# Optimization experiments

Measured on AMD Instinct MI355X. Metric: run time of the kernel, lower is better.

## Reference

```python
import jax, jax.numpy as jnp
import numpy as np

SR = 44100
LOWEST_HZ = 55.0
N_FRAMES = 100
L_ORDER = 5                       # l_filter_order
NC = L_ORDER + 1                  # num_coefficients
NA = L_ORDER + 2                  # num_active_indexes
V = int(SR // LOWEST_HZ) + NA     # coeff_vector_size = 808
N_SAMPLES = 44100


def _nat_cubic_spline_eval(y, t_out):
    """Natural cubic spline through y (n_knots, d) on uniform knots in [0,1],
    evaluated at t_out (T,). Returns (T, d)."""
    n, d = y.shape
    h = 1.0 / (n - 1)
    # second derivatives M: natural BC -> M[0] = M[n-1] = 0, tridiagonal solve
    rhs = 6.0 * (y[2:] - 2.0 * y[1:-1] + y[:-2]) / h        # (n-2, d)
    T = (jnp.diag(jnp.full((n - 2,), 4.0 * h))
         + jnp.diag(jnp.full((n - 3,), h), 1)
         + jnp.diag(jnp.full((n - 3,), h), -1))
    M_in = jnp.linalg.solve(T, rhs)
    M = jnp.concatenate([jnp.zeros((1, d), y.dtype), M_in, jnp.zeros((1, d), y.dtype)])
    idx = jnp.clip((t_out / h).astype(jnp.int32), 0, n - 2)
    f = (t_out - idx.astype(y.dtype) * h)[:, None]          # fractional offset
    y0, y1 = y[idx], y[idx + 1]
    M0, M1 = M[idx], M[idx + 1]
    bcoef = (y1 - y0) / h - h * (2.0 * M0 + M1) / 6.0
    ccoef = 0.5 * M0
    dcoef = (M1 - M0) / (6.0 * h)
    return y0 + f * (bcoef + f * (ccoef + f * dcoef))


def _sample_wise_lpc(x, a):
    """Time-varying all-pole filter: y[t] = x[t] - sum_i a[t, i] * y[t-1-i].
    x: (T,), a: (T, p) -> y: (T,)."""
    p = a.shape[1]

    def step(hist, inp):
        xt, at = inp
        yt = xt - jnp.dot(at, hist)
        hist = jnp.concatenate([yt[None], hist[:-1]])
        return hist, yt

    _, y = jax.lax.scan(step, jnp.zeros((p,), x.dtype), (x, a))
    return y


def setup_inputs() -> dict:
    key = jax.random.key(0)
    k1, k2, k3, k4 = jax.random.split(key, 4)
    # delay in samples, ~[300, 500] -> f0 in [88, 147] Hz, safely inside V=808
    delay_len_frames = 300.0 + 200.0 * jax.random.uniform(k1, (N_FRAMES,), dtype=jnp.float32)
    raw_gain = jnp.full((1,), 2.5, jnp.float32)             # sigmoid -> ~0.924 loop gain
    # raw coeffs uniform in (-2, 0) like the torch init
    raw_coeff_frames = -2.0 * jax.random.uniform(k2, (N_FRAMES, NC), dtype=jnp.float32)
    excitation = jax.random.normal(k3, (N_SAMPLES,), dtype=jnp.float32)
    exc_coefficients = 0.01 * jax.random.normal(k4, (1, N_SAMPLES, 1), dtype=jnp.float32)
    return {"delay_len_frames": delay_len_frames, "raw_gain": raw_gain,
            "raw_coeff_frames": raw_coeff_frames, "excitation": excitation,
            "exc_coefficients": exc_coefficients, "n_samples": N_SAMPLES}


def reference(delay_len_frames, raw_gain, raw_coeff_frames, excitation,
              exc_coefficients, n_samples):
    # constrained, normalized loop-filter coefficients per frame
    gain = jax.nn.sigmoid(raw_gain)                          # (1,)
    sig = jax.nn.sigmoid(raw_coeff_frames)                   # (F, NC)
    b_frames = sig / jnp.sum(sig, -1, keepdims=True) * gain

    # upsample delay + coeffs jointly with one natural cubic spline
    params = jnp.concatenate([delay_len_frames[:, None], b_frames], axis=1)  # (F, NC+1)
    t_out = jnp.linspace(0.0, 1.0, n_samples)
    up = _nat_cubic_spline_eval(params, t_out)               # (T, NC+1)
    delay, b = up[:, 0], up[:, 1:]

    z = jnp.floor(delay).astype(jnp.int32)                   # integer delay
    alfa = delay - jnp.floor(delay)                          # fractional part

    # scatter-build the per-sample sparse filter rows into dense A (T, V)
    cols = z[:, None] + jnp.arange(NA)[None, :]              # (T, NA)
    first = (-(1.0 - alfa) * b[:, 0])[:, None]
    mid = -(alfa[:, None] * b[:, :-1] + (1.0 - alfa)[:, None] * b[:, 1:])
    last = (-alfa * b[:, -1])[:, None]
    vals = jnp.concatenate([first, mid, last], axis=1)       # (T, NA)
    A = jnp.zeros((n_samples, V), jnp.float32).at[
        jnp.arange(n_samples)[:, None], cols].set(vals)

    # excitation shaping (order-1 time-varying all-pole), then KS string loop
    x = _sample_wise_lpc(excitation, exc_coefficients[0])
    y = _sample_wise_lpc(x, A)
    return y
```

## Files before the change

### kernel.cpp

```cpp
#include <hip/hip_runtime.h>

#define NSMP 44100
#define NKNOT 100
#define NIV  (NKNOT - 1)
#define NCC 6
#define NAA 7
#define RING 1024
#define NTH 320
#define SEG ((NSMP + NTH - 1) / NTH)
#define GW 8
#define WS_NEEDED ((size_t)NSMP * 32)

__device__ __forceinline__ float sigm(float x) { return 1.0f / (1.0f + expf(-x)); }

__device__ __forceinline__ void lean_barrier() {
    asm volatile("s_waitcnt lgkmcnt(0)" ::: "memory");
    __builtin_amdgcn_s_barrier();
    __builtin_amdgcn_sched_barrier(0);
}

__device__ __forceinline__ void prep_spline(
    const float* __restrict__ dlf, const float* __restrict__ rg,
    const float* __restrict__ rcf,
    float (*P)[NAA], float (*M)[NAA], float* CPs, float* IMs,
    float4 (*CO)[8], int* s_minz, int tid)
{
    const float H = 1.0f / 99.0f;
    if (tid < NKNOT) {
        float g = sigm(rg[0]);
        float s[NCC];
        float sum = 0.0f;
#pragma unroll
        for (int j = 0; j < NCC; ++j) { s[j] = sigm(rcf[tid * NCC + j]); sum += s[j]; }
        P[tid][0] = dlf[tid];
#pragma unroll
        for (int j = 0; j < NCC; ++j) P[tid][j + 1] = s[j] / sum * g;
    }
    if (tid < NKNOT - 2) {
        float cp = 0.25f;
        int n = tid; if (n > 10) n = 10;
        for (int k = 0; k < n; ++k) cp = 1.0f / (4.0f - cp);
        CPs[tid] = cp;
    }
    __syncthreads();
    if (tid >= 1 && tid < NKNOT - 2) IMs[tid] = 99.0f / (4.0f - CPs[tid - 1]);
    __syncthreads();
    if (tid < NAA) {
        int c = tid;
        float rhs0  = 6.0f * (P[2][c] - 2.0f * P[1][c] + P[0][c]) * 99.0f;
        float dprev = rhs0 * 24.75f;
        M[1][c] = dprev;
        for (int i = 1; i < NKNOT - 2; ++i) {
            float rhs = 6.0f * (P[i + 2][c] - 2.0f * P[i + 1][c] + P[i][c]) * 99.0f;
            float d   = (rhs - H * dprev) * IMs[i];
            M[i + 1][c] = d;
            dprev = d;
        }
        float nxt = M[NKNOT - 2][c];
        for (int i = NKNOT - 4; i >= 0; --i) {
            float v = M[i + 1][c] - CPs[i] * nxt;
            M[i + 1][c] = v;
            nxt = v;
        }
        M[0][c] = 0.0f;
        M[NKNOT - 1][c] = 0.0f;
    }
    __syncthreads();
    if (tid < NIV) {
        float lb = fminf(P[tid][0], P[tid + 1][0])
                 - (H * H * 0.125f) * fmaxf(fabsf(M[tid][0]), fabsf(M[tid + 1][0]));
        atomicMin(s_minz, (int)floorf(lb));
    }
    for (int iv = tid; iv < NIV; iv += blockDim.x) {
#pragma unroll
        for (int c = 0; c < NAA; ++c) {
            float y0 = P[iv][c], y1 = P[iv + 1][c];
            float m0 = M[iv][c], m1 = M[iv + 1][c];
            float b  = (y1 - y0) * 99.0f - H * (2.0f * m0 + m1) * (1.0f / 6.0f);
            CO[iv][c] = make_float4(y0, b, 0.5f * m0, (m1 - m0) * (99.0f / 6.0f));
        }
    }
    __syncthreads();
}


__global__ __launch_bounds__(NTH, 1) void diffks_fast(
    const float* __restrict__ dlf, const float* __restrict__ rg,
    const float* __restrict__ rcf, const float* __restrict__ exc,
    const float* __restrict__ ecoef, float* __restrict__ out,
    float4* __restrict__ recA, float4* __restrict__ recB)
{
    __shared__ float  P[NKNOT][NAA];
    __shared__ float  M[NKNOT][NAA];
    __shared__ float4 CO[NIV][8];
    __shared__ float  ring[2 * RING];
    __shared__ float  CPs[NKNOT - 2];
    __shared__ float  IMs[NKNOT - 2];
    __shared__ float  wpS[NTH / 64], wqS[NTH / 64];
    __shared__ int    s_minz;

    const int tid  = threadIdx.x;
    const int lane = tid & 63;
    const int wav  = tid >> 6;
    const float H   = 1.0f / 99.0f;
    const float INV = 1.0f / (float)(NSMP - 1);

    if (tid == 0) s_minz = 0x7fffffff;
    for (int i = tid; i < 2 * RING; i += NTH) ring[i] = 0.0f;

    prep_spline(dlf, rg, rcf, P, M, CPs, IMs, CO, &s_minz, tid);

    {
        int start = tid * SEG;
        int end   = min(start + SEG, NSMP);
        int cidx = -1;
        float4 k0, k1, k2, k3, k4, k5, k6;
        k0 = k1 = k2 = k3 = k4 = k5 = k6 = make_float4(0.f, 0.f, 0.f, 0.f);
        for (int t = start; t < end; ++t) {
            float tt = (float)t * INV;
            int idx = (int)(tt * 99.0f); if (idx > NIV - 1) idx = NIV - 1;
            if (idx != cidx) {
                k0 = CO[idx][0]; k1 = CO[idx][1]; k2 = CO[idx][2]; k3 = CO[idx][3];
                k4 = CO[idx][4]; k5 = CO[idx][5]; k6 = CO[idx][6];
                cidx = idx;
            }
            float f = tt - (float)idx * H;
            float r0 = k0.x + f * (k0.y + f * (k0.z + f * k0.w));
            float r1 = k1.x + f * (k1.y + f * (k1.z + f * k1.w));
            float r2 = k2.x + f * (k2.y + f * (k2.z + f * k2.w));
            float r3 = k3.x + f * (k3.y + f * (k3.z + f * k3.w));
            float r4 = k4.x + f * (k4.y + f * (k4.z + f * k4.w));
            float r5 = k5.x + f * (k5.y + f * (k5.z + f * k5.w));
            float r6 = k6.x + f * (k6.y + f * (k6.z + f * k6.w));
            float fl = floorf(r0);
            float alfa = r0 - fl, om = 1.0f - alfa;
            float w6 = -om * r1;
            float w5 = -(alfa * r1 + om * r2);
            float w4 = -(alfa * r2 + om * r3);
            float w3 = -(alfa * r3 + om * r4);
            float w2 = -(alfa * r4 + om * r5);
            float w1 = -(alfa * r5 + om * r6);
            float w0 = -alfa * r6;
            int ra = (t - 1 - (int)fl - 6) & (RING - 1);
            recA[t] = make_float4(w0, w1, w2, w3);
            recB[t] = make_float4(w4, w5, w6, __int_as_float(ra));
        }
    }

    {
        int start = tid * SEG;
        int end   = min(start + SEG, NSMP);
        float p = 1.0f, q = 0.0f;
#pragma unroll 4
        for (int t = start; t < end; ++t) {
            float a2 = ecoef[t];
            q = fmaf(-a2, q, exc[t]);
            p *= -a2;
        }
#pragma unroll
        for (int d = 1; d < 64; d <<= 1) {
            float pp = __shfl_up(p, d);
            float qq = __shfl_up(q, d);
            if (lane >= d) { q = fmaf(p, qq, q); p *= pp; }
        }
        if (lane == 63) { wpS[wav] = p; wqS[wav] = q; }
        float pe = __shfl_up(p, 1);
        float qe = __shfl_up(q, 1);
        if (lane == 0) { pe = 1.0f; qe = 0.0f; }
        __syncthreads();
        float v = 0.0f;
        for (int w = 0; w < wav; ++w) v = fmaf(wpS[w], v, wqS[w]);
        float y = fmaf(pe, v, qe);
#pragma unroll 4
        for (int t = start; t < end; ++t) {
            y = fmaf(-ecoef[t], y, exc[t]);
            out[t] = y;
        }
    }
    __syncthreads();

    int C = s_minz + 1;
    if (C > NTH) C = NTH;
    if (C < 1)  C = 1;
    const int NW   = (NSMP + C - 1) / C;
    const int NCH  = (NW + GW - 1) / GW;
    const int step = GW * C;

    float4 qa[GW], qb[GW];
    float  xs[GW];
#pragma unroll
    for (int g = 0; g < GW; ++g) {
        int t = g * C + tid;
        bool a = (tid < C) && (t < NSMP);
        int tc = a ? t : 0;
        qa[g] = recA[tc];
        qb[g] = recB[tc];
        xs[g] = a ? out[t] : 0.0f;
    }

    for (int ch = 0; ch < NCH; ++ch) {
        const int W0 = ch * step;
        float4 na[GW], nb[GW];
        float  nx[GW];
#pragma unroll
        for (int g = 0; g < GW; ++g) {
            int tn = W0 + step + g * C + tid;
            bool an = (tid < C) && (tn < NSMP);
            int tc = an ? tn : 0;
            na[g] = recA[tc];
            nb[g] = recB[tc];
            nx[g] = an ? out[tc] : 0.0f;
        }
#pragma unroll
        for (int g = 0; g < GW; ++g) {
            int t = W0 + g * C + tid;
            bool a = (tid < C) && (t < NSMP);
            int ra = __float_as_int(qb[g].w);
            const float* rp = &ring[(unsigned)ra];
            float y0 = rp[0], y1 = rp[1], y2 = rp[2], y3 = rp[3];
            float y4 = rp[4], y5 = rp[5], y6 = rp[6];
            float s = ((qa[g].x * y0 + qa[g].y * y1) + (qa[g].z * y2 + qa[g].w * y3))
                    + ((qb[g].x * y4 + qb[g].y * y5) + qb[g].z * y6);
            float acc = xs[g] - s;
            if (a) {
                int wi = t & (RING - 1);
                ring[wi]        = acc;
                ring[wi + RING] = acc;
                out[t] = acc;
            }
            lean_barrier();
        }
#pragma unroll
        for (int g = 0; g < GW; ++g) { qa[g] = na[g]; qb[g] = nb[g]; xs[g] = nx[g]; }
    }
}


#define FNTH 320
#define FSEG ((NSMP + FNTH - 1) / FNTH)
#define FGW 8

__device__ __forceinline__ void compute_rec_f(const float4 (*CO)[8], int t, bool a,
                                              float* wr, int* raOut) {
    const float H   = 1.0f / 99.0f;
    const float INV = 1.0f / (float)(NSMP - 1);
    if (!a) {
#pragma unroll
        for (int d = 0; d < NAA; ++d) wr[d] = 0.0f;
        *raOut = 0;
        return;
    }
    float tt = (float)t * INV;
    int idx = (int)(tt * 99.0f); if (idx > NIV - 1) idx = NIV - 1;
    float f = tt - (float)idx * H;
    float r[NAA];
#pragma unroll
    for (int c = 0; c < NAA; ++c) {
        float4 k = CO[idx][c];
        r[c] = k.x + f * (k.y + f * (k.z + f * k.w));
    }
    float fl = floorf(r[0]);
    float alfa = r[0] - fl, om = 1.0f - alfa;
    wr[6] = -om * r[1];
    wr[5] = -(alfa * r[1] + om * r[2]);
    wr[4] = -(alfa * r[2] + om * r[3]);
    wr[3] = -(alfa * r[3] + om * r[4]);
    wr[2] = -(alfa * r[4] + om * r[5]);
    wr[1] = -(alfa * r[5] + om * r[6]);
    wr[0] = -alfa * r[6];
    *raOut = (t - 1 - (int)fl - 6) & (RING - 1);
}

__global__ __launch_bounds__(FNTH, 1) void diffks_fallback(
    const float* __restrict__ dlf, const float* __restrict__ rg,
    const float* __restrict__ rcf, const float* __restrict__ exc,
    const float* __restrict__ ecoef, float* __restrict__ out)
{
    __shared__ float  P[NKNOT][NAA];
    __shared__ float  M[NKNOT][NAA];
    __shared__ float4 CO[NIV][8];
    __shared__ float  ring[2 * RING];
    __shared__ float  CPs[NKNOT - 2];
    __shared__ float  IMs[NKNOT - 2];
    __shared__ float  wpS[FNTH / 64], wqS[FNTH / 64];
    __shared__ int    s_minz;

    const int tid  = threadIdx.x;
    const int lane = tid & 63;
    const int wav  = tid >> 6;

    if (tid == 0) s_minz = 0x7fffffff;
    for (int i = tid; i < 2 * RING; i += FNTH) ring[i] = 0.0f;

    prep_spline(dlf, rg, rcf, P, M, CPs, IMs, CO, &s_minz, tid);

    {
        int start = tid * FSEG;
        int end   = min(start + FSEG, NSMP);
        float p = 1.0f, q = 0.0f;
#pragma unroll 4
        for (int t = start; t < end; ++t) {
            float a2 = ecoef[t];
            q = fmaf(-a2, q, exc[t]);
            p *= -a2;
        }
#pragma unroll
        for (int d = 1; d < 64; d <<= 1) {
            float pp = __shfl_up(p, d);
            float qq = __shfl_up(q, d);
            if (lane >= d) { q = fmaf(p, qq, q); p *= pp; }
        }
        if (lane == 63) { wpS[wav] = p; wqS[wav] = q; }
        float pe = __shfl_up(p, 1);
        float qe = __shfl_up(q, 1);
        if (lane == 0) { pe = 1.0f; qe = 0.0f; }
        __syncthreads();
        float v = 0.0f;
        for (int w = 0; w < wav; ++w) v = fmaf(wpS[w], v, wqS[w]);
        float y = fmaf(pe, v, qe);
#pragma unroll 4
        for (int t = start; t < end; ++t) {
            y = fmaf(-ecoef[t], y, exc[t]);
            out[t] = y;
        }
    }
    __syncthreads();

    int C = s_minz + 1;
    if (C > FNTH) C = FNTH;
    if (C < 1)  C = 1;
    const int NW   = (NSMP + C - 1) / C;
    const int NCH  = (NW + FGW - 1) / FGW;
    const int step = FGW * C;

    float  wA[FGW][NAA];
    int    raA[FGW];
    float  xsA[FGW];
    int    wiA[FGW];
    bool   aA[FGW];
    float* opA[FGW];
#pragma unroll
    for (int g = 0; g < FGW; ++g) {
        int t = g * C + tid;
        bool a = (tid < C) && (t < NSMP);
        compute_rec_f(CO, t, a, wA[g], &raA[g]);
        xsA[g]  = a ? out[t] : 0.0f;
        wiA[g]  = t & (RING - 1);
        aA[g]   = a;
        opA[g]  = out + t;
    }
    for (int ch = 0; ch < NCH; ++ch) {
        const int Wn = (ch + 1) * step;
        float  nx[FGW]; int ntv[FGW]; int nwi[FGW]; bool nav[FGW]; float* nop[FGW];
#pragma unroll
        for (int g = 0; g < FGW; ++g) {
            int tn = Wn + g * C + tid;
            bool an = (tid < C) && (tn < NSMP);
            nx[g]  = an ? out[tn] : 0.0f;
            ntv[g] = tn; nwi[g] = tn & (RING - 1); nav[g] = an; nop[g] = out + tn;
        }
        float wB[FGW][NAA]; int raB[FGW];
#pragma unroll
        for (int g = 0; g < FGW; ++g) {
            const float* rp = &ring[(unsigned)raA[g]];
            float y0 = rp[0], y1 = rp[1], y2 = rp[2], y3 = rp[3];
            float y4 = rp[4], y5 = rp[5], y6 = rp[6];
            compute_rec_f(CO, ntv[g], nav[g], wB[g], &raB[g]);
            float s = ((wA[g][0] * y0 + wA[g][1] * y1) + (wA[g][2] * y2 + wA[g][3] * y3))
                    + ((wA[g][4] * y4 + wA[g][5] * y5) + wA[g][6] * y6);
            float acc = xsA[g] - s;
            if (aA[g]) {
                ring[wiA[g]] = acc;
                ring[wiA[g] + RING] = acc;
                *opA[g] = acc;
            }
            lean_barrier();
        }
#pragma unroll
        for (int g = 0; g < FGW; ++g) {
#pragma unroll
            for (int d = 0; d < NAA; ++d) wA[g][d] = wB[g][d];
            raA[g] = raB[g]; xsA[g] = nx[g]; wiA[g] = nwi[g];
            aA[g] = nav[g]; opA[g] = nop[g];
        }
    }
}

extern "C" void kernel_launch(void* const* d_in, const int* in_sizes, int n_in,
                              void* d_out, int out_size, void* d_ws, size_t ws_size,
                              hipStream_t stream) {
    const float* dlf   = (const float*)d_in[0];
    const float* rg    = (const float*)d_in[1];
    const float* rcf   = (const float*)d_in[2];
    const float* exc   = (const float*)d_in[3];
    const float* ecoef = (const float*)d_in[4];
    float* out = (float*)d_out;

    if (d_ws != nullptr && ws_size >= WS_NEEDED) {
        float4* recA = (float4*)d_ws;
        float4* recB = (float4*)((char*)d_ws + (size_t)NSMP * 16);
        hipLaunchKernelGGL(diffks_fast, dim3(1), dim3(NTH), 0, stream,
                           dlf, rg, rcf, exc, ecoef, out, recA, recB);
    } else {
        hipLaunchKernelGGL(diffks_fallback, dim3(1), dim3(FNTH), 0, stream,
                           dlf, rg, rcf, exc, ecoef, out);
    }
}
```

Before: 151.5 us.

## Process three samples per thread on two waves in the KS wavefront loop

```diff
diff --git a/kernel.cpp b/kernel.cpp
--- a/kernel.cpp
+++ b/kernel.cpp
@@ -8,7 +8,6 @@
 #define RING 1024
 #define NTH 320
 #define SEG ((NSMP + NTH - 1) / NTH)
-#define GW 8
 #define WS_NEEDED ((size_t)NSMP * 32)
 
 __device__ __forceinline__ float sigm(float x) { return 1.0f / (1.0f + expf(-x)); }
@@ -180,58 +179,94 @@
     __syncthreads();
 
     int C = s_minz + 1;
-    if (C > NTH) C = NTH;
+    if (C > 384) C = 384;
     if (C < 1)  C = 1;
-    const int NW   = (NSMP + C - 1) / C;
-    const int NCH  = (NW + GW - 1) / GW;
-    const int step = GW * C;
-
-    float4 qa[GW], qb[GW];
-    float  xs[GW];
-#pragma unroll
-    for (int g = 0; g < GW; ++g) {
-        int t = g * C + tid;
-        bool a = (tid < C) && (t < NSMP);
-        int tc = a ? t : 0;
-        qa[g] = recA[tc];
-        qb[g] = recB[tc];
-        xs[g] = a ? out[t] : 0.0f;
-    }
-
-    for (int ch = 0; ch < NCH; ++ch) {
-        const int W0 = ch * step;
-        float4 na[GW], nb[GW];
-        float  nx[GW];
-#pragma unroll
-        for (int g = 0; g < GW; ++g) {
-            int tn = W0 + step + g * C + tid;
-            bool an = (tid < C) && (tn < NSMP);
-            int tc = an ? tn : 0;
-            na[g] = recA[tc];
-            nb[g] = recB[tc];
-            nx[g] = an ? out[tc] : 0.0f;
-        }
-#pragma unroll
-        for (int g = 0; g < GW; ++g) {
-            int t = W0 + g * C + tid;
-            bool a = (tid < C) && (t < NSMP);
-            int ra = __float_as_int(qb[g].w);
-            const float* rp = &ring[(unsigned)ra];
-            float y0 = rp[0], y1 = rp[1], y2 = rp[2], y3 = rp[3];
-            float y4 = rp[4], y5 = rp[5], y6 = rp[6];
-            float s = ((qa[g].x * y0 + qa[g].y * y1) + (qa[g].z * y2 + qa[g].w * y3))
-                    + ((qb[g].x * y4 + qb[g].y * y5) + qb[g].z * y6);
-            float acc = xs[g] - s;
-            if (a) {
-                int wi = t & (RING - 1);
-                ring[wi]        = acc;
-                ring[wi + RING] = acc;
-                out[t] = acc;
+    const int NW = (NSMP + C - 1) / C;
+    const bool busy = (tid < 128);
+
+    float4 a0, a1, a2c, b0, b1, b2c;
+    float  x0, x1, x2v;
+    a0 = a1 = a2c = b0 = b1 = b2c = make_float4(0.f, 0.f, 0.f, 0.f);
+    x0 = x1 = x2v = 0.0f;
+
+    const int s0 = tid;
+    const int s1 = 128 + tid;
+    const int s2 = 256 + tid;
+
+    if (busy) {
+        int u0 = s0, u1 = s1, u2 = s2;
+        int c0 = (s0 < C && u0 < NSMP) ? u0 : 0;
+        int c1 = (s1 < C && u1 < NSMP) ? u1 : 0;
+        int c2 = (s2 < C && u2 < NSMP) ? u2 : 0;
+        a0 = recA[c0]; b0 = recB[c0]; x0  = out[c0];
+        a1 = recA[c1]; b1 = recB[c1]; x1  = out[c1];
+        a2c = recA[c2]; b2c = recB[c2]; x2v = out[c2];
+    }
+
+#pragma unroll 1
+    for (int w = 0; w < NW; ++w) {
+        float4 na0, na1, na2, nb0, nb1, nb2;
+        float  nx0, nx1, nx2;
+        na0 = na1 = na2 = nb0 = nb1 = nb2 = make_float4(0.f, 0.f, 0.f, 0.f);
+        nx0 = nx1 = nx2 = 0.0f;
+        if (busy) {
+            const int tw = (w + 1) * C;
+            int u0 = tw + s0, u1 = tw + s1, u2 = tw + s2;
+            int c0 = (s0 < C && u0 < NSMP) ? u0 : 0;
+            int c1 = (s1 < C && u1 < NSMP) ? u1 : 0;
+            int c2 = (s2 < C && u2 < NSMP) ? u2 : 0;
+            na0 = recA[c0]; nb0 = recB[c0]; nx0 = out[c0];
+            na1 = recA[c1]; nb1 = recB[c1]; nx1 = out[c1];
+            na2 = recA[c2]; nb2 = recB[c2]; nx2 = out[c2];
+
+            const int tb = w * C;
+            {
+                const float* rp = &ring[(unsigned)__float_as_int(b0.w)];
+                float y0 = rp[0], y1 = rp[1], y2 = rp[2], y3 = rp[3];
+                float y4 = rp[4], y5 = rp[5], y6 = rp[6];
+                float s = ((a0.x * y0 + a0.y * y1) + (a0.z * y2 + a0.w * y3))
+                        + ((b0.x * y4 + b0.y * y5) + b0.z * y6);
+                float acc = x0 - s;
+                int t = tb + s0;
+                if (s0 < C && t < NSMP) {
+                    int wi = t & (RING - 1);
+                    ring[wi] = acc; ring[wi + RING] = acc;
+                    out[t] = acc;
+                }
             }
-            lean_barrier();
-        }
-#pragma unroll
-        for (int g = 0; g < GW; ++g) { qa[g] = na[g]; qb[g] = nb[g]; xs[g] = nx[g]; }
+            {
+                const float* rp = &ring[(unsigned)__float_as_int(b1.w)];
+                float y0 = rp[0], y1 = rp[1], y2 = rp[2], y3 = rp[3];
+                float y4 = rp[4], y5 = rp[5], y6 = rp[6];
+                float s = ((a1.x * y0 + a1.y * y1) + (a1.z * y2 + a1.w * y3))
+                        + ((b1.x * y4 + b1.y * y5) + b1.z * y6);
+                float acc = x1 - s;
+                int t = tb + s1;
+                if (s1 < C && t < NSMP) {
+                    int wi = t & (RING - 1);
+                    ring[wi] = acc; ring[wi + RING] = acc;
+                    out[t] = acc;
+                }
+            }
+            {
+                const float* rp = &ring[(unsigned)__float_as_int(b2c.w)];
+                float y0 = rp[0], y1 = rp[1], y2 = rp[2], y3 = rp[3];
+                float y4 = rp[4], y5 = rp[5], y6 = rp[6];
+                float s = ((a2c.x * y0 + a2c.y * y1) + (a2c.z * y2 + a2c.w * y3))
+                        + ((b2c.x * y4 + b2c.y * y5) + b2c.z * y6);
+                float acc = x2v - s;
+                int t = tb + s2;
+                if (s2 < C && t < NSMP) {
+                    int wi = t & (RING - 1);
+                    ring[wi] = acc; ring[wi + RING] = acc;
+                    out[t] = acc;
+                }
+            }
+        }
+        lean_barrier();
+        a0 = na0; b0 = nb0; x0 = nx0;
+        a1 = na1; b1 = nb1; x1 = nx1;
+        a2c = na2; b2c = nb2; x2v = nx2;
     }
 }
 
```

Result: slower. 205.3 us (+35.5%).

## Run KS recurrence wavefront in a single wave without block barriers

Applied to the files above, without the earlier changes.

```diff
diff --git a/kernel.cpp b/kernel.cpp
--- a/kernel.cpp
+++ b/kernel.cpp
@@ -8,7 +8,6 @@
 #define RING 1024
 #define NTH 320
 #define SEG ((NSMP + NTH - 1) / NTH)
-#define GW 8
 #define WS_NEEDED ((size_t)NSMP * 32)
 
 __device__ __forceinline__ float sigm(float x) { return 1.0f / (1.0f + expf(-x)); }
@@ -179,59 +178,54 @@
     }
     __syncthreads();
 
+    if (tid >= 64) return;
+
     int C = s_minz + 1;
-    if (C > NTH) C = NTH;
+    if (C > 320) C = 320;
     if (C < 1)  C = 1;
-    const int NW   = (NSMP + C - 1) / C;
-    const int NCH  = (NW + GW - 1) / GW;
-    const int step = GW * C;
-
-    float4 qa[GW], qb[GW];
-    float  xs[GW];
-#pragma unroll
-    for (int g = 0; g < GW; ++g) {
-        int t = g * C + tid;
-        bool a = (tid < C) && (t < NSMP);
-        int tc = a ? t : 0;
-        qa[g] = recA[tc];
-        qb[g] = recB[tc];
-        xs[g] = a ? out[t] : 0.0f;
-    }
-
-    for (int ch = 0; ch < NCH; ++ch) {
-        const int W0 = ch * step;
-        float4 na[GW], nb[GW];
-        float  nx[GW];
-#pragma unroll
-        for (int g = 0; g < GW; ++g) {
-            int tn = W0 + step + g * C + tid;
-            bool an = (tid < C) && (tn < NSMP);
-            int tc = an ? tn : 0;
-            na[g] = recA[tc];
-            nb[g] = recB[tc];
-            nx[g] = an ? out[tc] : 0.0f;
-        }
-#pragma unroll
-        for (int g = 0; g < GW; ++g) {
-            int t = W0 + g * C + tid;
-            bool a = (tid < C) && (t < NSMP);
-            int ra = __float_as_int(qb[g].w);
-            const float* rp = &ring[(unsigned)ra];
+    const int NW = (NSMP + C - 1) / C;
+
+    float4 a[5], b[5];
+    float  x[5];
+#pragma unroll
+    for (int r = 0; r < 5; ++r) {
+        int pos = r * 64 + lane;
+        int tc = (pos < C) ? pos : 0;
+        a[r] = recA[tc]; b[r] = recB[tc]; x[r] = out[tc];
+    }
+
+#pragma unroll 1
+    for (int w = 0; w < NW; ++w) {
+        float4 na[5], nb[5];
+        float  nx[5];
+#pragma unroll
+        for (int r = 0; r < 5; ++r) {
+            int pos = r * 64 + lane;
+            int t = (w + 1) * C + pos;
+            int tc = (pos < C && t < NSMP) ? t : 0;
+            na[r] = recA[tc]; nb[r] = recB[tc]; nx[r] = out[tc];
+        }
+#pragma unroll
+        for (int r = 0; r < 5; ++r) {
+            int pos = r * 64 + lane;
+            int t = w * C + pos;
+            const float* rp = &ring[(unsigned)__float_as_int(b[r].w)];
             float y0 = rp[0], y1 = rp[1], y2 = rp[2], y3 = rp[3];
             float y4 = rp[4], y5 = rp[5], y6 = rp[6];
-            float s = ((qa[g].x * y0 + qa[g].y * y1) + (qa[g].z * y2 + qa[g].w * y3))
-                    + ((qb[g].x * y4 + qb[g].y * y5) + qb[g].z * y6);
-            float acc = xs[g] - s;
-            if (a) {
+            float s = ((a[r].x * y0 + a[r].y * y1) + (a[r].z * y2 + a[r].w * y3))
+                    + ((b[r].x * y4 + b[r].y * y5) + b[r].z * y6);
+            float acc = x[r] - s;
+            if (pos < C && t < NSMP) {
                 int wi = t & (RING - 1);
                 ring[wi]        = acc;
                 ring[wi + RING] = acc;
                 out[t] = acc;
             }
-            lean_barrier();
-        }
-#pragma unroll
-        for (int g = 0; g < GW; ++g) { qa[g] = na[g]; qb[g] = nb[g]; xs[g] = nx[g]; }
+        }
+        asm volatile("s_waitcnt lgkmcnt(0)" ::: "memory");
+        __builtin_amdgcn_sched_barrier(0);
+#pragma unroll
+        for (int r = 0; r < 5; ++r) { a[r] = na[r]; b[r] = nb[r]; x[r] = nx[r]; }
     }
 }
 
```

New measurement: 244.0 us, median of 4. 1.61x slower.
